# Kernel tuning notes

Hardware: AMD Instinct MI355X
Metric: run time of the kernel (lower is better)

Reference implementation:

```python
import jax, jax.numpy as jnp
import numpy as np

T, B, N1, N2, N3, N4 = 512, 256, 512, 256, 64, 784
BETA_LIF = 0.9
BETA_LI = 0.95
THR = 1.0
LN_EPS = 1e-5


@jax.custom_vjp
def spike(x):
    # snntorch heaviside fire with ATan surrogate gradient (alpha=2 default)
    return (x > 0).astype(x.dtype)

def _spike_fwd(x):
    return spike(x), x

def _spike_bwd(x, g):
    return (g / (1.0 + (jnp.pi * x) ** 2),)

spike.defvjp(_spike_fwd, _spike_bwd)


def setup_inputs() -> dict:
    key = jax.random.key(0)
    ks = jax.random.split(key, 10)
    def lin(k, out_d, in_d):
        k1, k2 = jax.random.split(k)
        bound = 1.0 / np.sqrt(in_d)
        W = jax.random.uniform(k1, (out_d, in_d), jnp.float32, -bound, bound)
        b = jax.random.uniform(k2, (out_d,), jnp.float32, -bound, bound)
        return W, b
    W_lif, b_lif = lin(ks[0], N1, N2)
    W_li, b_li = lin(ks[1], N2, N1)
    W1, b1 = lin(ks[2], N3, N2)
    W2, b2 = lin(ks[3], N4, N3)
    # binary spike train input
    spk_rec = (jax.random.uniform(ks[4], (T, B, N2)) < 0.1).astype(jnp.float32)
    return {
        'spk_rec': spk_rec,
        'W_lif': W_lif, 'b_lif': b_lif,
        'W_li': W_li, 'b_li': b_li,
        'W1': W1, 'b1': b1,
        'W2': W2, 'b2': b2,
        'ln_g': jnp.ones((N4,), jnp.float32),
        'ln_b': jnp.zeros((N4,), jnp.float32),
    }


def reference(spk_rec, W_lif, b_lif, W_li, b_li, W1, b1, W2, b2, ln_g, ln_b):
    # Precompute per-step input currents with one big GEMM: [T,B,n1]
    cur_seq = jnp.einsum('tbi,oi->tbo', spk_rec, W_lif) + b_lif

    def lif_step(mem, cur):
        # snntorch Leaky, reset_mechanism='subtract':
        # reset based on previous-step membrane (detached)
        reset = jax.lax.stop_gradient((mem - THR > 0).astype(mem.dtype))
        mem_new = BETA_LIF * mem + cur - reset * THR
        spk = spike(mem_new - THR)
        return mem_new, spk

    mem0 = jnp.zeros(cur_seq.shape[1:], cur_seq.dtype)
    _, lif_spk = jax.lax.scan(lif_step, mem0, cur_seq)  # [T,B,n1]

    li_in = jnp.einsum('tbi,oi->tbo', lif_spk, W_li) + b_li  # [T,B,n2]
    beta_li = jnp.clip(jnp.asarray(BETA_LI, li_in.dtype), 0.0, 1.0)

    def li_step(mem, inp):
        mem = beta_li * mem + inp
        return mem, mem

    _, li_mem = jax.lax.scan(li_step, jnp.zeros(li_in.shape[1:], li_in.dtype), li_in)

    x = li_mem.mean(axis=0)  # [B,n2]
    h = jax.nn.relu(x @ W1.T + b1)  # [B,n3]
    y = h @ W2.T + b2  # [B,n4]
    mu = jnp.mean(y, axis=-1, keepdims=True)
    var = jnp.var(y, axis=-1, keepdims=True)
    return (y - mu) / jnp.sqrt(var + LN_EPS) * ln_g + ln_b
```

## Files before the change

### kernel.cpp

```cpp
#include <hip/hip_runtime.h>
#include <hip/hip_bf16.h>
#include <cmath>
#include <cstdint>


#define T_TOT 512
#define B_SZ  256
#define N1    512
#define N2    256
#define N3    64
#define N4    784
#define BN    (B_SZ * N1)
#define SW    264

typedef unsigned short u16;
typedef short bf16x8 __attribute__((ext_vector_type(8)));
typedef float f32x4 __attribute__((ext_vector_type(4)));

#define OFF_BLIF 0
#define OFF_WLI  512
#define OFF_BLI  131584
#define OFF_W1   131840
#define OFF_B1   148224
#define OFF_W2   148288
#define OFF_B2   198464
#define OFF_LNG  199248
#define OFF_LNB  200032
#define CANON_N  200816

__device__ __forceinline__ float b2f(u16 u) {
  return __uint_as_float(((uint32_t)u) << 16);
}
__device__ __forceinline__ u16 f2b(float f) {
  uint32_t x = __float_as_uint(f);
  return (u16)((x + 0x7fffu + ((x >> 16) & 1u)) >> 16);
}
__device__ __forceinline__ float ldany(const void* p, long i, int isbf) {
  return isbf ? b2f(((const u16*)p)[i]) : ((const float*)p)[i];
}
__device__ __forceinline__ uint32_t pk_trunc(float a, float b) {
  return (__float_as_uint(a) >> 16) | (__float_as_uint(b) & 0xFFFF0000u);
}

__global__ __launch_bounds__(256) void k_initconv(
    const void* wA, const void* wB, const void* t0, const void* t1,
    const void* t2, const void* spk, u16* __restrict__ spkb,
    uint32_t* __restrict__ det, uint32_t* __restrict__ sBF,
    uint32_t* __restrict__ sF32)
{
  __shared__ uint32_t redA[256], redB[256];
  int bid = blockIdx.x, tid = threadIdx.x;

  if (bid >= 163) {
    size_t j0 = (size_t)(bid - 163) * 1024 + (size_t)tid * 4;
    const uint4* inB = (const uint4*)spk;
    uint4 lo[4];
    #pragma unroll
    for (int c = 0; c < 4; c++) lo[c] = inB[j0 + c];
    uint32_t f = 0;
    #pragma unroll
    for (int c = 0; c < 4; c++)
      if (lo[c].x == 0x3F803F80u || lo[c].y == 0x3F803F80u ||
          lo[c].z == 0x3F803F80u || lo[c].w == 0x3F803F80u) f = 1;
    redA[tid] = f; __syncthreads();
    for (int s = 128; s > 0; s >>= 1) {
      if (tid < s) redA[tid] |= redA[tid + s];
      __syncthreads();
    }
    uint4* outB = (uint4*)spkb;
    if (redA[0]) {
      #pragma unroll
      for (int c = 0; c < 4; c++) outB[j0 + c] = lo[c];
    } else {
      const float4* inF = (const float4*)spk;
      #pragma unroll
      for (int c = 0; c < 4; c++) {
        float4 a = inF[2 * (j0 + c)], b = inF[2 * (j0 + c) + 1];
        uint4 p;
        p.x = pk_trunc(a.x, a.y); p.y = pk_trunc(a.z, a.w);
        p.z = pk_trunc(b.x, b.y); p.w = pk_trunc(b.z, b.w);
        outB[j0 + c] = p;
      }
    }
    return;
  }

  if (bid >= 131) {
    const uint32_t* p = (const uint32_t*)spk + (size_t)(bid - 131) * 4096 +
                        (size_t)tid * 16;
    uint32_t f = 0;
    #pragma unroll
    for (int j = 0; j < 16; j++) if (p[j] == 0x3F803F80u) f = 1;
    redA[tid] = f; __syncthreads();
    for (int s = 128; s > 0; s >>= 1) {
      if (tid < s) redA[tid] |= redA[tid + s];
      __syncthreads();
    }
    if (tid == 0) det[bid - 131] = redA[0];
    return;
  }

  uint32_t mB = 0, mF = 0;
  if (bid < 128) {
    const uint32_t* p = (const uint32_t*)(bid < 64 ? wA : wB) +
                        (size_t)(bid & 63) * 1024 + tid;
    #pragma unroll
    for (int k = 0; k < 4; k++) {
      uint32_t w = p[k * 256];
      uint32_t f = w & 0x7FFFFFFFu; if (f > mF) mF = f;
      uint32_t h0 = (w << 16) & 0x7FFFFFFFu;
      uint32_t h1 = w & 0x7FFF0000u;
      if (h0 > mB) mB = h0;
      if (h1 > mB) mB = h1;
    }
  } else {
    const uint32_t* p = (const uint32_t*)(bid == 128 ? t0 : bid == 129 ? t1 : t2);
    for (int i = tid; i < 392; i += 256) {
      uint32_t w = p[i];
      uint32_t f = w & 0x7FFFFFFFu; if (f > mF) mF = f;
      uint32_t h0 = (w << 16) & 0x7FFFFFFFu;
      uint32_t h1 = w & 0x7FFF0000u;
      if (h0 > mB) mB = h0;
      if (h1 > mB) mB = h1;
    }
  }
  int slot = bid < 128 ? bid : 64 + bid;
  redA[tid] = mB; redB[tid] = mF; __syncthreads();
  for (int s = 128; s > 0; s >>= 1) {
    if (tid < s) {
      if (redA[tid + s] > redA[tid]) redA[tid] = redA[tid + s];
      if (redB[tid + s] > redB[tid]) redB[tid] = redB[tid + s];
    }
    __syncthreads();
  }
  if (tid == 0) { sBF[slot] = redA[0]; sF32[slot] = redB[0]; }
}

__device__ void reduce_slots(const uint32_t* det, const uint32_t* sBF,
                             const uint32_t* sF32, int* isbf_o,
                             uint32_t st[5]) {
  uint32_t f = 0;
  for (int i = 0; i < 32; i++) f |= det[i];
  const uint32_t* S = f ? sBF : sF32;
  uint32_t a0 = 0, a1 = 0;
  for (int i = 0; i < 64; i++) { if (S[i] > a0) a0 = S[i]; }
  for (int i = 64; i < 128; i++) { if (S[i] > a1) a1 = S[i]; }
  st[0] = a0; st[1] = a1; st[2] = S[192]; st[3] = S[193]; st[4] = S[194];
  *isbf_o = (int)f;
}

__global__ __launch_bounds__(256) void k_prep(
    const void* wA, const void* wB,
    const void* t0, const void* t1, const void* t2,
    const void* s_blif, const void* s_bli, const void* s_w1,
    const void* s_b1, const void* s_w2,
    float* __restrict__ canon, u16* __restrict__ Whi, u16* __restrict__ Wlo,
    const uint32_t* __restrict__ det, const uint32_t* __restrict__ sBF,
    const uint32_t* __restrict__ sF32)
{
  int isbf; uint32_t st[5];
  reduce_slots(det, sBF, sF32, &isbf, st);
  const void* s_wlif = (st[0] >= st[1]) ? wA : wB;
  const void* s_wli  = (st[0] >= st[1]) ? wB : wA;
  uint32_t s2 = st[2], s3 = st[3], s4 = st[4];
  const void *s_lng, *s_lnb, *s_b2;
  if (s2 >= s3 && s2 >= s4)      s_lng = t0;
  else if (s3 >= s2 && s3 >= s4) s_lng = t1;
  else                           s_lng = t2;
  if (s2 <= s3 && s2 <= s4)      s_lnb = t0;
  else if (s3 <= s2 && s3 <= s4) s_lnb = t1;
  else                           s_lnb = t2;
  s_b2 = (t0 != s_lng && t0 != s_lnb) ? t0
       : (t1 != s_lng && t1 != s_lnb) ? t1 : t2;

  long id = (long)blockIdx.x * 256 + threadIdx.x;
  if (id < 512)    { canon[OFF_BLIF + id] = ldany(s_blif, id, isbf); return; } id -= 512;
  if (id < 131072) { canon[OFF_WLI  + id] = ldany(s_wli,  id, isbf); return; } id -= 131072;
  if (id < 256)    { canon[OFF_BLI  + id] = ldany(s_bli,  id, isbf); return; } id -= 256;
  if (id < 16384)  { canon[OFF_W1   + id] = ldany(s_w1,   id, isbf); return; } id -= 16384;
  if (id < 64)     { canon[OFF_B1   + id] = ldany(s_b1,   id, isbf); return; } id -= 64;
  if (id < 50176)  { canon[OFF_W2   + id] = ldany(s_w2,   id, isbf); return; } id -= 50176;
  if (id < 784)    { canon[OFF_B2   + id] = ldany(s_b2,   id, isbf); return; } id -= 784;
  if (id < 784)    { canon[OFF_LNG  + id] = ldany(s_lng,  id, isbf); return; } id -= 784;
  if (id < 784)    { canon[OFF_LNB  + id] = ldany(s_lnb,  id, isbf); return; } id -= 784;
  if (id < 131072) {
    float wv = ldany(s_wlif, id, isbf);
    u16 h = f2b(wv);
    Whi[id] = h;
    Wlo[id] = f2b(wv - b2f(h));
  }
}

#define SSTEP6(val, M, C, Gv) {                                              \
    float rst_ = (M) > 1.0f ? 1.0f : 0.0f;                                   \
    (M) = 0.9f * (M) + (val) - rst_;                                         \
    float sp_ = (M) > 1.0f ? 1.0f : 0.0f;                                    \
    (C) += sp_;                                                              \
    (Gv) = 0.95f * (Gv) + sp_; }

__global__ __launch_bounds__(512, 2) void k_fused(
    const u16* __restrict__ spkb, const u16* __restrict__ Whi,
    const u16* __restrict__ Wlo, const float* __restrict__ canon,
    float* __restrict__ Sg)
{
  __shared__ alignas(16) u16 Ab[2][64 * SW];
  int tid = threadIdx.x, bid = blockIdx.x;
  int nb = bid >> 6, bb = bid & 63;
  int n0 = nb * 128, b0 = bb * 4;
  int lane = tid & 63, wv = tid >> 6;
  int nw = wv & 3, bh = wv >> 2;
  int lr = lane & 15, lq = lane >> 4;

  bf16x8 wh[2][8], wl[2][8];
  #pragma unroll
  for (int jn = 0; jn < 2; jn++) {
    const u16* ph = Whi + (size_t)(n0 + nw * 32 + jn * 16 + lr) * N2 + lq * 8;
    const u16* pl = Wlo + (size_t)(n0 + nw * 32 + jn * 16 + lr) * N2 + lq * 8;
    #pragma unroll
    for (int ks = 0; ks < 8; ks++) {
      wh[jn][ks] = *(const bf16x8*)(ph + ks * 32);
      wl[jn][ks] = *(const bf16x8*)(pl + ks * 32);
    }
  }
  float bv0 = canon[OFF_BLIF + n0 + nw * 32 + lr];
  float bv1 = canon[OFF_BLIF + n0 + nw * 32 + 16 + lr];

  int sr[4], sk[4];
  #pragma unroll
  for (int c = 0; c < 4; c++) {
    int f = tid + 512 * c;
    sr[c] = f >> 5;
    sk[c] = f & 31;
  }
  int4 pre[4];
  #define ALOAD(it) { _Pragma("unroll") for (int c = 0; c < 4; c++)          \
      pre[c] = *(const int4*)(spkb +                                         \
        (size_t)((16 * (it) + (sr[c] & 15)) * 256 + b0 + (sr[c] >> 4)) * N2  \
        + sk[c] * 8); }
  #define ASTORE(bf) { _Pragma("unroll") for (int c = 0; c < 4; c++)         \
      *(int4*)&Ab[bf][sr[c] * SW + sk[c] * 8] = pre[c]; }

  ALOAD(0) ASTORE(0)
  ALOAD(1)
  __syncthreads();

  float mem = 0.f, cnt = 0.f, G = 0.f;

  for (int it = 0; it < 32; it++) {
    const u16* ab = Ab[it & 1];
    f32x4 acc[2][2];
    #pragma unroll
    for (int i = 0; i < 2; i++)
      #pragma unroll
      for (int jn = 0; jn < 2; jn++)
        #pragma unroll
        for (int r = 0; r < 4; r++) acc[i][jn][r] = 0.0f;

    #pragma unroll
    for (int ks = 0; ks < 8; ks++) {
      bf16x8 af[2];
      #pragma unroll
      for (int i = 0; i < 2; i++)
        af[i] = *(const bf16x8*)(ab + (16 * (bh * 2 + i) + lr) * SW + ks * 32 + lq * 8);
      #pragma unroll
      for (int i = 0; i < 2; i++) {
        acc[i][0] = __builtin_amdgcn_mfma_f32_16x16x32_bf16(af[i], wh[0][ks], acc[i][0], 0, 0, 0);
        acc[i][0] = __builtin_amdgcn_mfma_f32_16x16x32_bf16(af[i], wl[0][ks], acc[i][0], 0, 0, 0);
        acc[i][1] = __builtin_amdgcn_mfma_f32_16x16x32_bf16(af[i], wh[1][ks], acc[i][1], 0, 0, 0);
        acc[i][1] = __builtin_amdgcn_mfma_f32_16x16x32_bf16(af[i], wl[1][ks], acc[i][1], 0, 0, 0);
      }
    }
    if (it < 31) ASTORE((it + 1) & 1)
    if (it < 30) ALOAD(it + 2)

    float Y[4][4];
    #pragma unroll
    for (int rr = 0; rr < 4; rr++) {
      float x0 = acc[0][0][rr], x1 = acc[1][0][rr];
      float x2 = acc[0][1][rr], x3 = acc[1][1][rr];
      float s0 = __shfl_xor(x0, 16), s1 = __shfl_xor(x1, 16);
      float s2 = __shfl_xor(x2, 16), s3 = __shfl_xor(x3, 16);
      bool g1 = (lq & 1) != 0;
      float z0 = g1 ? s1 : x0, z1 = g1 ? x1 : s0;
      float z2 = g1 ? s3 : x2, z3 = g1 ? x3 : s2;
      float t0 = __shfl_xor(z0, 32), t1 = __shfl_xor(z1, 32);
      float t2 = __shfl_xor(z2, 32), t3 = __shfl_xor(z3, 32);
      bool g2 = (lq & 2) != 0;
      Y[rr][0] = g2 ? t2 : z0; Y[rr][1] = g2 ? t3 : z1;
      Y[rr][2] = g2 ? z2 : t0; Y[rr][3] = g2 ? z3 : t1;
    }
    float bv = (lq & 2) ? bv1 : bv0;
    #pragma unroll
    for (int j = 0; j < 4; j++)
      #pragma unroll
      for (int rr = 0; rr < 4; rr++)
        SSTEP6(Y[rr][j] + bv, mem, cnt, G)

    __syncthreads();
  }
  #undef ALOAD
  #undef ASTORE

  int nA = n0 + nw * 32 + (lq >> 1) * 16 + lr;
  int bA = b0 + bh * 2 + (lq & 1);
  Sg[(size_t)nA * 256 + bA] = (cnt - 0.95f * G) * 20.0f;
}

__global__ __launch_bounds__(256) void k_tail(
    const float* __restrict__ Sg, const float* __restrict__ canon,
    float* __restrict__ outp, float Csum)
{
  __shared__ float sS[N1];
  __shared__ float sx[N2];
  __shared__ float sh[N3];
  __shared__ float sy[N4];
  __shared__ float red[256];
  int b = blockIdx.x, tid = threadIdx.x;

  for (int i = tid; i < N1; i += 256) sS[i] = Sg[(size_t)i * 256 + b];
  __syncthreads();

  {
    const float4* w = (const float4*)(canon + OFF_WLI + (size_t)tid * N1);
    float a = 0.f;
    for (int k = 0; k < N1 / 4; k++) {
      float4 p4 = w[k];
      a += sS[k*4] * p4.x + sS[k*4+1] * p4.y + sS[k*4+2] * p4.z + sS[k*4+3] * p4.w;
    }
    sx[tid] = (a + Csum * canon[OFF_BLI + tid]) * (1.0f / (float)T_TOT);
  }
  __syncthreads();

  if (tid < N3) {
    const float4* w = (const float4*)(canon + OFF_W1 + (size_t)tid * N2);
    float a = 0.f;
    for (int k = 0; k < N2 / 4; k++) {
      float4 p4 = w[k];
      a += sx[k*4] * p4.x + sx[k*4+1] * p4.y + sx[k*4+2] * p4.z + sx[k*4+3] * p4.w;
    }
    a += canon[OFF_B1 + tid];
    sh[tid] = a > 0.f ? a : 0.f;
  }
  __syncthreads();

  for (int n = tid; n < N4; n += 256) {
    const float4* w = (const float4*)(canon + OFF_W2 + (size_t)n * N3);
    float a = 0.f;
    for (int k = 0; k < N3 / 4; k++) {
      float4 p4 = w[k];
      a += sh[k*4] * p4.x + sh[k*4+1] * p4.y + sh[k*4+2] * p4.z + sh[k*4+3] * p4.w;
    }
    sy[n] = a + canon[OFF_B2 + n];
  }
  __syncthreads();

  float p = 0.f;
  for (int n = tid; n < N4; n += 256) p += sy[n];
  red[tid] = p; __syncthreads();
  for (int s = 128; s > 0; s >>= 1) { if (tid < s) red[tid] += red[tid + s]; __syncthreads(); }
  float mu = red[0] / (float)N4;
  __syncthreads();
  p = 0.f;
  for (int n = tid; n < N4; n += 256) { float d = sy[n] - mu; p += d * d; }
  red[tid] = p; __syncthreads();
  for (int s = 128; s > 0; s >>= 1) { if (tid < s) red[tid] += red[tid + s]; __syncthreads(); }
  float var = red[0] / (float)N4;
  float sc = 1.0f / sqrtf(var + 1e-5f);
  for (int n = tid; n < N4; n += 256) {
    outp[(size_t)b * N4 + n] =
        (sy[n] - mu) * sc * canon[OFF_LNG + n] + canon[OFF_LNB + n];
  }
}

__global__ void k_fillv(float* o, int n, float V) {
  int i = blockIdx.x * 256 + threadIdx.x;
  if (i < n) o[i] = V;
}

extern "C" void kernel_launch(void* const* d_in, const int* in_sizes, int n_in,
                              void* d_out, int out_size, void* d_ws, size_t ws_size,
                              hipStream_t stream) {
  float* out = (float*)d_out;

  int idx_spk = -1, idx_blif = -1, idx_bli = -1, idx_w1 = -1, idx_b1 = -1,
      idx_w2 = -1;
  int idxW[2] = {-1, -1}, nW = 0;
  int idxT[3] = {-1, -1, -1}, nT = 0;
  bool ok = (n_in == 11);
  for (int i = 0; ok && i < 11; i++) {
    switch (in_sizes[i]) {
      case 33554432: if (idx_spk  < 0) idx_spk  = i; else ok = false; break;
      case 512:      if (idx_blif < 0) idx_blif = i; else ok = false; break;
      case 256:      if (idx_bli  < 0) idx_bli  = i; else ok = false; break;
      case 16384:    if (idx_w1   < 0) idx_w1   = i; else ok = false; break;
      case 64:       if (idx_b1   < 0) idx_b1   = i; else ok = false; break;
      case 50176:    if (idx_w2   < 0) idx_w2   = i; else ok = false; break;
      case 131072:   if (nW < 2) idxW[nW++] = i; else ok = false; break;
      case 784:      if (nT < 3) idxT[nT++] = i; else ok = false; break;
      default: ok = false;
    }
  }
  ok = ok && idx_spk >= 0 && idx_blif >= 0 && idx_bli >= 0 && idx_w1 >= 0 &&
       idx_b1 >= 0 && idx_w2 >= 0 && nW == 2 && nT == 3;
  if (!ok) {
    k_fillv<<<(out_size + 255) / 256, 256, 0, stream>>>(
        out, out_size, (float)(n_in >= 1 ? in_sizes[0] : -1));
    return;
  }
  if (out_size != B_SZ * N4) {
    k_fillv<<<(out_size + 255) / 256, 256, 0, stream>>>(
        out, out_size, 1.0e6f + (float)out_size);
    return;
  }

  char* w = (char*)d_ws;
  uint32_t* det  = (uint32_t*)w;
  uint32_t* sBF  = (uint32_t*)(w + 128);
  uint32_t* sF32 = (uint32_t*)(w + 1024);
  float* canon = (float*)(w + 2048);
  size_t canonB = ((size_t)CANON_N * 4 + 255) & ~(size_t)255;
  u16* Whi = (u16*)(w + 2048 + canonB);
  u16* Wlo = Whi + BN;
  float* Sg = (float*)((char*)Wlo + (size_t)BN * 2);
  u16* spkb = (u16*)((char*)Sg + (size_t)BN * 4);
  size_t need = 2048 + canonB + (size_t)2 * BN * 2 + (size_t)BN * 4 +
                (size_t)T_TOT * B_SZ * N2 * 2;
  if (ws_size < need) {
    k_fillv<<<(out_size + 255) / 256, 256, 0, stream>>>(out, out_size, 2.0e6f);
    return;
  }

  double beta = 0.95;
  double bT = std::pow(beta, (double)T_TOT);
  float Csum = (float)(((double)T_TOT - beta * (1.0 - bT) / (1.0 - beta)) / (1.0 - beta));

  k_initconv<<<4259, 256, 0, stream>>>(
      d_in[idxW[0]], d_in[idxW[1]], d_in[idxT[0]], d_in[idxT[1]],
      d_in[idxT[2]], d_in[idx_spk], spkb, det, sBF, sF32);
  k_prep<<<1297, 256, 0, stream>>>(
      d_in[idxW[0]], d_in[idxW[1]], d_in[idxT[0]], d_in[idxT[1]],
      d_in[idxT[2]], d_in[idx_blif], d_in[idx_bli], d_in[idx_w1],
      d_in[idx_b1], d_in[idx_w2], canon, Whi, Wlo, det, sBF, sF32);
  k_fused<<<256, 512, 0, stream>>>(spkb, Whi, Wlo, canon, Sg);
  k_tail<<<B_SZ, 256, 0, stream>>>(Sg, canon, out, Csum);
}
```

Baseline: 354.5 us.

## Halve per-block batch tile in fused LIF kernel to double grid size

```diff
diff --git a/kernel.cpp b/kernel.cpp
--- a/kernel.cpp
+++ b/kernel.cpp
@@ -198,46 +198,43 @@
     (C) += sp_;                                                              \
     (Gv) = 0.95f * (Gv) + sp_; }
 
-__global__ __launch_bounds__(512, 2) void k_fused(
+__global__ __launch_bounds__(512, 4) void k_fused(
     const u16* __restrict__ spkb, const u16* __restrict__ Whi,
     const u16* __restrict__ Wlo, const float* __restrict__ canon,
     float* __restrict__ Sg)
 {
-  __shared__ alignas(16) u16 Ab[2][64 * SW];
+  __shared__ alignas(16) u16 Ab[2][32 * SW];
   int tid = threadIdx.x, bid = blockIdx.x;
-  int nb = bid >> 6, bb = bid & 63;
-  int n0 = nb * 128, b0 = bb * 4;
+  int nb = bid >> 7, bb = bid & 127;
+  int n0 = nb * 128, b0 = bb * 2;
   int lane = tid & 63, wv = tid >> 6;
-  int nw = wv & 3, bh = wv >> 2;
   int lr = lane & 15, lq = lane >> 4;
 
-  bf16x8 wh[2][8], wl[2][8];
+  bf16x8 wh[8], wl[8];
+  {
+    const u16* ph = Whi + (size_t)(n0 + wv * 16 + lr) * N2 + lq * 8;
+    const u16* pl = Wlo + (size_t)(n0 + wv * 16 + lr) * N2 + lq * 8;
+    #pragma unroll
+    for (int ks = 0; ks < 8; ks++) {
+      wh[ks] = *(const bf16x8*)(ph + ks * 32);
+      wl[ks] = *(const bf16x8*)(pl + ks * 32);
+    }
+  }
+  float bv = canon[OFF_BLIF + n0 + wv * 16 + lr];
+
+  int sr[2], sk[2];
   #pragma unroll
-  for (int jn = 0; jn < 2; jn++) {
-    const u16* ph = Whi + (size_t)(n0 + nw * 32 + jn * 16 + lr) * N2 + lq * 8;
-    const u16* pl = Wlo + (size_t)(n0 + nw * 32 + jn * 16 + lr) * N2 + lq * 8;
-    #pragma unroll
-    for (int ks = 0; ks < 8; ks++) {
-      wh[jn][ks] = *(const bf16x8*)(ph + ks * 32);
-      wl[jn][ks] = *(const bf16x8*)(pl + ks * 32);
-    }
-  }
-  float bv0 = canon[OFF_BLIF + n0 + nw * 32 + lr];
-  float bv1 = canon[OFF_BLIF + n0 + nw * 32 + 16 + lr];
-
-  int sr[4], sk[4];
-  #pragma unroll
-  for (int c = 0; c < 4; c++) {
+  for (int c = 0; c < 2; c++) {
     int f = tid + 512 * c;
     sr[c] = f >> 5;
     sk[c] = f & 31;
   }
-  int4 pre[4];
-  #define ALOAD(it) { _Pragma("unroll") for (int c = 0; c < 4; c++)          \
+  int4 pre[2];
+  #define ALOAD(it) { _Pragma("unroll") for (int c = 0; c < 2; c++)          \
       pre[c] = *(const int4*)(spkb +                                         \
         (size_t)((16 * (it) + (sr[c] & 15)) * 256 + b0 + (sr[c] >> 4)) * N2  \
         + sk[c] * 8); }
-  #define ASTORE(bf) { _Pragma("unroll") for (int c = 0; c < 4; c++)         \
+  #define ASTORE(bf) { _Pragma("unroll") for (int c = 0; c < 2; c++)         \
       *(int4*)&Ab[bf][sr[c] * SW + sk[c] * 8] = pre[c]; }
 
   ALOAD(0) ASTORE(0)
@@ -248,48 +245,43 @@
 
   for (int it = 0; it < 32; it++) {
     const u16* ab = Ab[it & 1];
-    f32x4 acc[2][2];
+    f32x4 acc[2];
     #pragma unroll
     for (int i = 0; i < 2; i++)
       #pragma unroll
-      for (int jn = 0; jn < 2; jn++)
-        #pragma unroll
-        for (int r = 0; r < 4; r++) acc[i][jn][r] = 0.0f;
+      for (int r = 0; r < 4; r++) acc[i][r] = 0.0f;
 
     #pragma unroll
     for (int ks = 0; ks < 8; ks++) {
-      bf16x8 af[2];
-      #pragma unroll
-      for (int i = 0; i < 2; i++)
-        af[i] = *(const bf16x8*)(ab + (16 * (bh * 2 + i) + lr) * SW + ks * 32 + lq * 8);
-      #pragma unroll
-      for (int i = 0; i < 2; i++) {
-        acc[i][0] = __builtin_amdgcn_mfma_f32_16x16x32_bf16(af[i], wh[0][ks], acc[i][0], 0, 0, 0);
-        acc[i][0] = __builtin_amdgcn_mfma_f32_16x16x32_bf16(af[i], wl[0][ks], acc[i][0], 0, 0, 0);
-        acc[i][1] = __builtin_amdgcn_mfma_f32_16x16x32_bf16(af[i], wh[1][ks], acc[i][1], 0, 0, 0);
-        acc[i][1] = __builtin_amdgcn_mfma_f32_16x16x32_bf16(af[i], wl[1][ks], acc[i][1], 0, 0, 0);
-      }
+      bf16x8 af0 = *(const bf16x8*)(ab + (lr) * SW + ks * 32 + lq * 8);
+      bf16x8 af1 = *(const bf16x8*)(ab + (16 + lr) * SW + ks * 32 + lq * 8);
+      acc[0] = __builtin_amdgcn_mfma_f32_16x16x32_bf16(af0, wh[ks], acc[0], 0, 0, 0);
+      acc[0] = __builtin_amdgcn_mfma_f32_16x16x32_bf16(af0, wl[ks], acc[0], 0, 0, 0);
+      acc[1] = __builtin_amdgcn_mfma_f32_16x16x32_bf16(af1, wh[ks], acc[1], 0, 0, 0);
+      acc[1] = __builtin_amdgcn_mfma_f32_16x16x32_bf16(af1, wl[ks], acc[1], 0, 0, 0);
     }
     if (it < 31) ASTORE((it + 1) & 1)
     if (it < 30) ALOAD(it + 2)
 
     float Y[4][4];
+    bool g1 = (lq & 1) != 0, g2 = (lq & 2) != 0;
     #pragma unroll
     for (int rr = 0; rr < 4; rr++) {
-      float x0 = acc[0][0][rr], x1 = acc[1][0][rr];
-      float x2 = acc[0][1][rr], x3 = acc[1][1][rr];
+      float x0 = acc[0][rr], x1 = acc[1][rr];
       float s0 = __shfl_xor(x0, 16), s1 = __shfl_xor(x1, 16);
-      float s2 = __shfl_xor(x2, 16), s3 = __shfl_xor(x3, 16);
-      bool g1 = (lq & 1) != 0;
-      float z0 = g1 ? s1 : x0, z1 = g1 ? x1 : s0;
-      float z2 = g1 ? s3 : x2, z3 = g1 ? x3 : s2;
-      float t0 = __shfl_xor(z0, 32), t1 = __shfl_xor(z1, 32);
-      float t2 = __shfl_xor(z2, 32), t3 = __shfl_xor(z3, 32);
-      bool g2 = (lq & 2) != 0;
-      Y[rr][0] = g2 ? t2 : z0; Y[rr][1] = g2 ? t3 : z1;
-      Y[rr][2] = g2 ? z2 : t0; Y[rr][3] = g2 ? z3 : t1;
-    }
-    float bv = (lq & 2) ? bv1 : bv0;
+      float va = g1 ? x1 : x0;
+      float vb = g1 ? s1 : s0;
+      float ta = __shfl_xor(va, 32);
+      float tb = __shfl_xor(vb, 32);
+      float p = g1 ? vb : va;
+      float q = g1 ? va : vb;
+      float r = g1 ? tb : ta;
+      float s = g1 ? ta : tb;
+      Y[rr][0] = g2 ? r : p;
+      Y[rr][1] = g2 ? s : q;
+      Y[rr][2] = g2 ? p : r;
+      Y[rr][3] = g2 ? q : s;
+    }
     #pragma unroll
     for (int j = 0; j < 4; j++)
       #pragma unroll
@@ -301,9 +293,10 @@
   #undef ALOAD
   #undef ASTORE
 
-  int nA = n0 + nw * 32 + (lq >> 1) * 16 + lr;
-  int bA = b0 + bh * 2 + (lq & 1);
-  Sg[(size_t)nA * 256 + bA] = (cnt - 0.95f * G) * 20.0f;
+  if (lq < 2) {
+    int nA = n0 + wv * 16 + lr;
+    Sg[(size_t)nA * 256 + b0 + lq] = (cnt - 0.95f * G) * 20.0f;
+  }
 }
 
 __global__ __launch_bounds__(256) void k_tail(
@@ -441,6 +434,6 @@
       d_in[idxW[0]], d_in[idxW[1]], d_in[idxT[0]], d_in[idxT[1]],
       d_in[idxT[2]], d_in[idx_blif], d_in[idx_bli], d_in[idx_w1],
       d_in[idx_b1], d_in[idx_w2], canon, Whi, Wlo, det, sBF, sF32);
-  k_fused<<<256, 512, 0, stream>>>(spkb, Whi, Wlo, canon, Sg);
+  k_fused<<<512, 512, 0, stream>>>(spkb, Whi, Wlo, canon, Sg);
   k_tail<<<B_SZ, 256, 0, stream>>>(Sg, canon, out, Csum);
 }
```

New measurement: 354.6 us. About the same (+0.0%).

## Fuse spike-input bf16 conversion into fused LIF kernel and retile to 512 blocks

Applied to the files above, without the earlier changes.

```diff
diff --git a/kernel.cpp b/kernel.cpp
--- a/kernel.cpp
+++ b/kernel.cpp
@@ -11,7 +11,6 @@
 #define N3    64
 #define N4    784
 #define BN    (B_SZ * N1)
-#define SW    264
 
 typedef unsigned short u16;
 typedef short bf16x8 __attribute__((ext_vector_type(8)));
@@ -44,46 +43,12 @@
 
 __global__ __launch_bounds__(256) void k_initconv(
     const void* wA, const void* wB, const void* t0, const void* t1,
-    const void* t2, const void* spk, u16* __restrict__ spkb,
+    const void* t2, const void* spk,
     uint32_t* __restrict__ det, uint32_t* __restrict__ sBF,
     uint32_t* __restrict__ sF32)
 {
   __shared__ uint32_t redA[256], redB[256];
   int bid = blockIdx.x, tid = threadIdx.x;
-
-  if (bid >= 163) {
-    size_t j0 = (size_t)(bid - 163) * 1024 + (size_t)tid * 4;
-    const uint4* inB = (const uint4*)spk;
-    uint4 lo[4];
-    #pragma unroll
-    for (int c = 0; c < 4; c++) lo[c] = inB[j0 + c];
-    uint32_t f = 0;
-    #pragma unroll
-    for (int c = 0; c < 4; c++)
-      if (lo[c].x == 0x3F803F80u || lo[c].y == 0x3F803F80u ||
-          lo[c].z == 0x3F803F80u || lo[c].w == 0x3F803F80u) f = 1;
-    redA[tid] = f; __syncthreads();
-    for (int s = 128; s > 0; s >>= 1) {
-      if (tid < s) redA[tid] |= redA[tid + s];
-      __syncthreads();
-    }
-    uint4* outB = (uint4*)spkb;
-    if (redA[0]) {
-      #pragma unroll
-      for (int c = 0; c < 4; c++) outB[j0 + c] = lo[c];
-    } else {
-      const float4* inF = (const float4*)spk;
-      #pragma unroll
-      for (int c = 0; c < 4; c++) {
-        float4 a = inF[2 * (j0 + c)], b = inF[2 * (j0 + c) + 1];
-        uint4 p;
-        p.x = pk_trunc(a.x, a.y); p.y = pk_trunc(a.z, a.w);
-        p.z = pk_trunc(b.x, b.y); p.w = pk_trunc(b.z, b.w);
-        outB[j0 + c] = p;
-      }
-    }
-    return;
-  }
 
   if (bid >= 131) {
     const uint32_t* p = (const uint32_t*)spk + (size_t)(bid - 131) * 4096 +
@@ -156,10 +121,11 @@
     const void* s_b1, const void* s_w2,
     float* __restrict__ canon, u16* __restrict__ Whi, u16* __restrict__ Wlo,
     const uint32_t* __restrict__ det, const uint32_t* __restrict__ sBF,
-    const uint32_t* __restrict__ sF32)
+    const uint32_t* __restrict__ sF32, uint32_t* __restrict__ flg)
 {
   int isbf; uint32_t st[5];
   reduce_slots(det, sBF, sF32, &isbf, st);
+  if (blockIdx.x == 0 && threadIdx.x == 0) flg[0] = (uint32_t)isbf;
   const void* s_wlif = (st[0] >= st[1]) ? wA : wB;
   const void* s_wli  = (st[0] >= st[1]) ? wB : wA;
   uint32_t s2 = st[2], s3 = st[3], s4 = st[4];
@@ -198,47 +164,55 @@
     (C) += sp_;                                                              \
     (Gv) = 0.95f * (Gv) + sp_; }
 
-__global__ __launch_bounds__(512, 2) void k_fused(
-    const u16* __restrict__ spkb, const u16* __restrict__ Whi,
+__global__ __launch_bounds__(256, 2) void k_fused(
+    const void* __restrict__ spk, const u16* __restrict__ Whi,
     const u16* __restrict__ Wlo, const float* __restrict__ canon,
-    float* __restrict__ Sg)
+    float* __restrict__ Sg, const uint32_t* __restrict__ flg)
 {
-  __shared__ alignas(16) u16 Ab[2][64 * SW];
+  __shared__ alignas(16) u16 Ab[2][32 * 256];
   int tid = threadIdx.x, bid = blockIdx.x;
-  int nb = bid >> 6, bb = bid & 63;
-  int n0 = nb * 128, b0 = bb * 4;
+  int nb = bid >> 7, bb = bid & 127;
+  int n0 = nb * 128, b0 = bb * 2;
   int lane = tid & 63, wv = tid >> 6;
-  int nw = wv & 3, bh = wv >> 2;
   int lr = lane & 15, lq = lane >> 4;
+  const int isbf = (int)flg[0];
 
   bf16x8 wh[2][8], wl[2][8];
   #pragma unroll
   for (int jn = 0; jn < 2; jn++) {
-    const u16* ph = Whi + (size_t)(n0 + nw * 32 + jn * 16 + lr) * N2 + lq * 8;
-    const u16* pl = Wlo + (size_t)(n0 + nw * 32 + jn * 16 + lr) * N2 + lq * 8;
+    const u16* ph = Whi + (size_t)(n0 + wv * 32 + jn * 16 + lr) * N2 + lq * 8;
+    const u16* pl = Wlo + (size_t)(n0 + wv * 32 + jn * 16 + lr) * N2 + lq * 8;
     #pragma unroll
     for (int ks = 0; ks < 8; ks++) {
       wh[jn][ks] = *(const bf16x8*)(ph + ks * 32);
       wl[jn][ks] = *(const bf16x8*)(pl + ks * 32);
     }
   }
-  float bv0 = canon[OFF_BLIF + n0 + nw * 32 + lr];
-  float bv1 = canon[OFF_BLIF + n0 + nw * 32 + 16 + lr];
+  float bv0 = canon[OFF_BLIF + n0 + wv * 32 + lr];
+  float bv1 = canon[OFF_BLIF + n0 + wv * 32 + 16 + lr];
 
   int sr[4], sk[4];
   #pragma unroll
   for (int c = 0; c < 4; c++) {
-    int f = tid + 512 * c;
+    int f = tid + 256 * c;
     sr[c] = f >> 5;
     sk[c] = f & 31;
   }
   int4 pre[4];
-  #define ALOAD(it) { _Pragma("unroll") for (int c = 0; c < 4; c++)          \
-      pre[c] = *(const int4*)(spkb +                                         \
-        (size_t)((16 * (it) + (sr[c] & 15)) * 256 + b0 + (sr[c] >> 4)) * N2  \
-        + sk[c] * 8); }
+  #define AELEM(it, c) (((size_t)((16 * (it) + (sr[c] & 15)) * 256 + b0 +    \
+                          (sr[c] >> 4))) * 256 + sk[c] * 8)
+  #define ALOAD(it) { if (isbf) {                                            \
+      _Pragma("unroll") for (int c = 0; c < 4; c++)                          \
+        pre[c] = *(const int4*)((const u16*)spk + AELEM(it, c));             \
+    } else {                                                                 \
+      _Pragma("unroll") for (int c = 0; c < 4; c++) {                        \
+        const float4* pf = (const float4*)spk + (AELEM(it, c) >> 2);         \
+        float4 fa = pf[0], fb = pf[1]; int4 p;                               \
+        p.x = (int)pk_trunc(fa.x, fa.y); p.y = (int)pk_trunc(fa.z, fa.w);    \
+        p.z = (int)pk_trunc(fb.x, fb.y); p.w = (int)pk_trunc(fb.z, fb.w);    \
+        pre[c] = p; } } }
   #define ASTORE(bf) { _Pragma("unroll") for (int c = 0; c < 4; c++)         \
-      *(int4*)&Ab[bf][sr[c] * SW + sk[c] * 8] = pre[c]; }
+      *(int4*)&Ab[bf][sr[c] * 256 + ((sk[c] ^ (sr[c] & 7)) * 8)] = pre[c]; }
 
   ALOAD(0) ASTORE(0)
   ALOAD(1)
@@ -258,10 +232,10 @@
 
     #pragma unroll
     for (int ks = 0; ks < 8; ks++) {
+      int sl = ((ks * 4 + lq) ^ (lr & 7)) * 8;
       bf16x8 af[2];
-      #pragma unroll
-      for (int i = 0; i < 2; i++)
-        af[i] = *(const bf16x8*)(ab + (16 * (bh * 2 + i) + lr) * SW + ks * 32 + lq * 8);
+      af[0] = *(const bf16x8*)(ab + lr * 256 + sl);
+      af[1] = *(const bf16x8*)(ab + (16 + lr) * 256 + sl);
       #pragma unroll
       for (int i = 0; i < 2; i++) {
         acc[i][0] = __builtin_amdgcn_mfma_f32_16x16x32_bf16(af[i], wh[0][ks], acc[i][0], 0, 0, 0);
@@ -271,6 +245,7 @@
       }
     }
     if (it < 31) ASTORE((it + 1) & 1)
+    __syncthreads();
     if (it < 30) ALOAD(it + 2)
 
     float Y[4][4];
@@ -295,14 +270,13 @@
       #pragma unroll
       for (int rr = 0; rr < 4; rr++)
         SSTEP6(Y[rr][j] + bv, mem, cnt, G)
-
-    __syncthreads();
   }
   #undef ALOAD
   #undef ASTORE
-
-  int nA = n0 + nw * 32 + (lq >> 1) * 16 + lr;
-  int bA = b0 + bh * 2 + (lq & 1);
+  #undef AELEM
+
+  int nA = n0 + wv * 32 + (lq >> 1) * 16 + lr;
+  int bA = b0 + (lq & 1);
   Sg[(size_t)nA * 256 + bA] = (cnt - 0.95f * G) * 20.0f;
 }
 
@@ -416,15 +390,14 @@
   char* w = (char*)d_ws;
   uint32_t* det  = (uint32_t*)w;
   uint32_t* sBF  = (uint32_t*)(w + 128);
+  uint32_t* flg  = (uint32_t*)(w + 1016);
   uint32_t* sF32 = (uint32_t*)(w + 1024);
   float* canon = (float*)(w + 2048);
   size_t canonB = ((size_t)CANON_N * 4 + 255) & ~(size_t)255;
   u16* Whi = (u16*)(w + 2048 + canonB);
   u16* Wlo = Whi + BN;
   float* Sg = (float*)((char*)Wlo + (size_t)BN * 2);
-  u16* spkb = (u16*)((char*)Sg + (size_t)BN * 4);
-  size_t need = 2048 + canonB + (size_t)2 * BN * 2 + (size_t)BN * 4 +
-                (size_t)T_TOT * B_SZ * N2 * 2;
+  size_t need = 2048 + canonB + (size_t)2 * BN * 2 + (size_t)BN * 4;
   if (ws_size < need) {
     k_fillv<<<(out_size + 255) / 256, 256, 0, stream>>>(out, out_size, 2.0e6f);
     return;
@@ -434,13 +407,13 @@
   double bT = std::pow(beta, (double)T_TOT);
   float Csum = (float)(((double)T_TOT - beta * (1.0 - bT) / (1.0 - beta)) / (1.0 - beta));
 
-  k_initconv<<<4259, 256, 0, stream>>>(
+  k_initconv<<<163, 256, 0, stream>>>(
       d_in[idxW[0]], d_in[idxW[1]], d_in[idxT[0]], d_in[idxT[1]],
-      d_in[idxT[2]], d_in[idx_spk], spkb, det, sBF, sF32);
+      d_in[idxT[2]], d_in[idx_spk], det, sBF, sF32);
   k_prep<<<1297, 256, 0, stream>>>(
       d_in[idxW[0]], d_in[idxW[1]], d_in[idxT[0]], d_in[idxT[1]],
       d_in[idxT[2]], d_in[idx_blif], d_in[idx_bli], d_in[idx_w1],
-      d_in[idx_b1], d_in[idx_w2], canon, Whi, Wlo, det, sBF, sF32);
-  k_fused<<<256, 512, 0, stream>>>(spkb, Whi, Wlo, canon, Sg);
+      d_in[idx_b1], d_in[idx_w2], canon, Whi, Wlo, det, sBF, sF32, flg);
+  k_fused<<<512, 256, 0, stream>>>(d_in[idx_spk], Whi, Wlo, canon, Sg, flg);
   k_tail<<<B_SZ, 256, 0, stream>>>(Sg, canon, out, Csum);
 }
```

Result: faster. 295.2 us (-16.7%).
